# Performance work log

Measured on AMD Instinct MI355X. Metric: run time of the kernel, lower is better.

## Reference

```python
import jax, jax.numpy as jnp
import numpy as np

N = 50000        # nodes
E = 800000       # edges
F_IN = 32        # float features (x also carries 1 trailing cell-id column)
CELL_DIM = 16
NUM_CELLS = 854
C = 64           # out_channels
H0, H1 = 2, 1    # heads schedule for num_layers=2 -> [2, 1]
D_IN = F_IN + CELL_DIM  # 48, GAT input dim after cell embedding concat
NEG_SLOPE = 0.2  # PyG GATConv default negative_slope


def setup_inputs() -> dict:
    key = jax.random.key(0)
    ks = jax.random.split(key, 14)
    base = jax.random.normal(ks[0], (N, F_IN), jnp.float32)
    cell_ids = jax.random.randint(ks[1], (N,), 0, NUM_CELLS)
    x = jnp.concatenate([base, cell_ids.astype(jnp.float32)[:, None]], axis=1)
    edge_index = jax.random.randint(ks[2], (2, E), 0, N, dtype=jnp.int32)
    s = lambda f: 1.0 / np.sqrt(f)
    emb = jax.random.normal(ks[3], (NUM_CELLS, CELL_DIM), jnp.float32)
    W0 = jax.random.normal(ks[4], (D_IN, H0 * C), jnp.float32) * s(D_IN)
    a_src0 = jax.random.normal(ks[5], (H0, C), jnp.float32) * s(C)
    a_dst0 = jax.random.normal(ks[6], (H0, C), jnp.float32) * s(C)
    b0 = jnp.zeros((C,), jnp.float32)
    ln_g = jnp.ones((C,), jnp.float32)
    ln_b = jnp.zeros((C,), jnp.float32)
    W1 = jax.random.normal(ks[7], (C, H1 * C), jnp.float32) * s(C)
    a_src1 = jax.random.normal(ks[8], (H1, C), jnp.float32) * s(C)
    a_dst1 = jax.random.normal(ks[9], (H1, C), jnp.float32) * s(C)
    b1 = jnp.zeros((C,), jnp.float32)
    return {"x": x, "edge_index": edge_index, "emb": emb,
            "W0": W0, "a_src0": a_src0, "a_dst0": a_dst0, "b0": b0,
            "ln_g": ln_g, "ln_b": ln_b,
            "W1": W1, "a_src1": a_src1, "a_dst1": a_dst1, "b1": b1}


def gat_layer(h_in, src, dst, W, a_src, a_dst, b, heads):
    # h_in: [N, D]; src/dst: [E'] (self-loops already appended)
    h = (h_in @ W).reshape(N, heads, C)                 # [N, H, C]
    alpha_s = jnp.einsum('nhc,hc->nh', h, a_src)        # [N, H]
    alpha_d = jnp.einsum('nhc,hc->nh', h, a_dst)
    e = jax.nn.leaky_relu(alpha_s[src] + alpha_d[dst], NEG_SLOPE)  # [E', H]
    # segment softmax over incoming edges of each dst node
    m = jax.ops.segment_max(e, dst, num_segments=N)     # [N, H]
    ex = jnp.exp(e - m[dst])
    denom = jax.ops.segment_sum(ex, dst, num_segments=N)
    alpha = ex / denom[dst]                             # [E', H]
    msg = h[src] * alpha[:, :, None]                    # [E', H, C]
    out = jax.ops.segment_sum(msg, dst, num_segments=N) # [N, H, C]
    return out.mean(axis=1) + b                         # concat=False -> mean over heads


def layer_norm(x, g, b):
    mu = x.mean(-1, keepdims=True)
    var = ((x - mu) ** 2).mean(-1, keepdims=True)
    return (x - mu) * jax.lax.rsqrt(var + 1e-5) * g + b


def reference(x, edge_index, emb, W0, a_src0, a_dst0, b0, ln_g, ln_b,
              W1, a_src1, a_dst1, b1):
    base = x[:, :-1]
    cell_ids = x[:, -1].astype(jnp.int32)
    h = jnp.concatenate([base, emb[cell_ids]], axis=1)  # [N, 48]
    # add self-loops (PyG GATConv default add_self_loops=True)
    loop = jnp.arange(N, dtype=edge_index.dtype)
    src = jnp.concatenate([edge_index[0], loop])
    dst = jnp.concatenate([edge_index[1], loop])
    h = gat_layer(h, src, dst, W0, a_src0, a_dst0, b0, H0)
    h = jax.nn.elu(layer_norm(h, ln_g, ln_b))           # dropout is identity at eval
    h = gat_layer(h, src, dst, W1, a_src1, a_dst1, b1, H1)
    return h
```

## Files before the change

kernel.cpp:

```cpp
#include <hip/hip_runtime.h>
#include <hip/hip_bf16.h>

#define N_NODES 50000
#define N_EDGES 800000
#define E_TOT 850000
#define F_IN 32
#define CELL_DIM 16
#define D_IN 48
#define X_STRIDE 33
#define NUM_CELLS 854
#define NEG_SLOPE 0.2f
#define SCAN_BLOCKS 49
#define NODE0_BLOCKS 2048
#define HIST_BLOCKS 3125

typedef unsigned int uint;
typedef unsigned short ushort;

static __device__ __forceinline__ uint f2b(float f) {
  uint x = __float_as_uint(f);
  return (x + 0x7fffu + ((x >> 16) & 1u)) >> 16;
}
static __device__ __forceinline__ float b2f_lo(uint w) { return __uint_as_float(w << 16); }
static __device__ __forceinline__ float b2f_hi(uint w) { return __uint_as_float(w & 0xffff0000u); }
static __device__ __forceinline__ float lrelu(float e) { return e > 0.f ? e : NEG_SLOPE * e; }


__global__ __launch_bounds__(256) void k_node0h(const float* __restrict__ x,
                                                const float* __restrict__ emb,
                                                const float* __restrict__ W0,
                                                const float* __restrict__ asrc,
                                                const float* __restrict__ adst,
                                                const int* __restrict__ ei,
                                                ushort* __restrict__ h0u,
                                                float* __restrict__ as0, float* __restrict__ ad0,
                                                int* __restrict__ deg) {
  int tid = threadIdx.x;
  if (blockIdx.x >= NODE0_BLOCKS) {
    int e = (blockIdx.x - NODE0_BLOCKS) * 256 + tid;
    if (e < N_EDGES) atomicAdd(&deg[ei[N_EDGES + e]], 1);
    return;
  }
  __shared__ float hin[8][48];
  int lane = tid & 63, wid = tid >> 6;
  int h = wid & 1;
  int q = wid >> 1;
  float w0r[D_IN];
#pragma unroll
  for (int k = 0; k < D_IN; ++k) w0r[k] = W0[k * 128 + h * 64 + lane];
  float av_s = asrc[h * 64 + lane], av_d = adst[h * 64 + lane];

  for (int g = blockIdx.x; g < N_NODES / 8; g += NODE0_BLOCKS) {
    int nb = g * 8;
#pragma unroll
    for (int j = 0; j < 2; ++j) {
      int loc = 2 * wid + j;
      int n = nb + loc;
      float t = 0.f;
      if (lane < 33) t = x[n * X_STRIDE + lane];
      int cid = (int)__shfl(t, 32, 64);
      cid = cid < 0 ? 0 : (cid >= NUM_CELLS ? NUM_CELLS - 1 : cid);
      if (lane >= 32 && lane < 48) t = emb[cid * CELL_DIM + (lane - 32)];
      if (lane < 48) hin[loc][lane] = t;
    }
    __syncthreads();
#pragma unroll
    for (int j = 0; j < 4; ++j) {
      int loc = 4 * q + j;
      int n = nb + loc;
      const float4* hp = (const float4*)hin[loc];
      float acc = 0.f;
#pragma unroll
      for (int k4 = 0; k4 < 12; ++k4) {
        float4 hh = hp[k4];
        acc = fmaf(hh.x, w0r[4 * k4 + 0], acc);
        acc = fmaf(hh.y, w0r[4 * k4 + 1], acc);
        acc = fmaf(hh.z, w0r[4 * k4 + 2], acc);
        acc = fmaf(hh.w, w0r[4 * k4 + 3], acc);
      }
      h0u[(n * 64 + lane) * 2 + h] = (ushort)f2b(acc);
      float sa = acc * av_s, sd = acc * av_d;
#pragma unroll
      for (int o = 32; o >= 1; o >>= 1) {
        sa += __shfl_xor(sa, o, 64);
        sd += __shfl_xor(sd, o, 64);
      }
      if (lane == 0) {
        as0[n * 2 + h] = sa;
        ad0[n * 2 + h] = sd;
      }
    }
    __syncthreads();
  }
}


__global__ __launch_bounds__(1024) void k_scan1(const int* __restrict__ deg, int* __restrict__ off,
                                                int* __restrict__ bsum) {
  __shared__ int ws[16];
  int tid = threadIdx.x;
  int lane = tid & 63, wid = tid >> 6;
  int i = blockIdx.x * 1024 + tid;
  int v = (i < N_NODES) ? deg[i] + 1 : 0;
  int sc = v;
#pragma unroll
  for (int o = 1; o < 64; o <<= 1) {
    int t = __shfl_up(sc, o, 64);
    if (lane >= o) sc += t;
  }
  if (lane == 63) ws[wid] = sc;
  __syncthreads();
  if (tid < 16) {
    int w = ws[tid];
    int s = w;
#pragma unroll
    for (int o = 1; o < 16; o <<= 1) {
      int t = __shfl_up(s, o, 64);
      if (tid >= o) s += t;
    }
    ws[tid] = s - w;
  }
  __syncthreads();
  int excl = sc - v + ws[wid];
  if (i < N_NODES) off[i] = excl;
  if (tid == 1023) bsum[blockIdx.x] = excl + v;
}

__global__ __launch_bounds__(1024) void k_scan23(int* __restrict__ off, int* __restrict__ ofs,
                                                 const int* __restrict__ bsum) {
  __shared__ int carry_s;
  int tid = threadIdx.x;
  if (tid < 64) {
    int v = (tid < SCAN_BLOCKS) ? bsum[tid] : 0;
    int s = v;
#pragma unroll
    for (int o = 1; o < 64; o <<= 1) {
      int t = __shfl_up(s, o, 64);
      if (tid >= o) s += t;
    }
    if (tid == (int)blockIdx.x) carry_s = s - v;
  }
  __syncthreads();
  int carry = carry_s;
  int i = blockIdx.x * 1024 + tid;
  if (i < N_NODES) {
    int v = off[i] + carry;
    off[i] = v;
    ofs[i] = v;
  }
  if (i == 0) off[N_NODES] = E_TOT;
}

__global__ __launch_bounds__(256) void k_scatter(const int* __restrict__ ei, int* __restrict__ ofs,
                                                 const int* __restrict__ off,
                                                 const float2* __restrict__ as0v,
                                                 const float2* __restrict__ ad0v,
                                                 uint2* __restrict__ ew) {
  int t = blockIdx.x * 256 + threadIdx.x;
  if (t < N_EDGES) {
    int s = ei[t], d = ei[N_EDGES + t];
    float2 a_s = as0v[s], a_d = ad0v[d];
    float w0 = __expf(lrelu(a_s.x + a_d.x));
    float w1 = __expf(lrelu(a_s.y + a_d.y));
    int p = atomicAdd(&ofs[d], 1);
    ew[p] = make_uint2((uint)s, f2b(w0) | (f2b(w1) << 16));
  } else if (t < N_EDGES + N_NODES) {
    int n = t - N_EDGES;
    int slot = off[n + 1] - 1;
    float2 a_s = as0v[n], a_d = ad0v[n];
    float w0 = __expf(lrelu(a_s.x + a_d.x));
    float w1 = __expf(lrelu(a_s.y + a_d.y));
    ew[slot] = make_uint2((uint)n, f2b(w0) | (f2b(w1) << 16));
  }
}


__global__ __launch_bounds__(256) void k_agg0(const int* __restrict__ off,
                                              const uint2* __restrict__ ew,
                                              const uint* __restrict__ h0p,
                                              const float* __restrict__ b0,
                                              const float* __restrict__ lng,
                                              const float* __restrict__ lnb,
                                              const float* __restrict__ W1,
                                              const float* __restrict__ asrc1,
                                              const float* __restrict__ adst1,
                                              ushort* __restrict__ h1b,
                                              float* __restrict__ as1, float* __restrict__ ad1) {
  int n = blockIdx.x * 4 + (threadIdx.x >> 6);
  int lane = threadIdx.x & 63;
  float acc0 = 0.f, acc1 = 0.f, den0 = 0.f, den1 = 0.f;
  int i0 = off[n], i1 = off[n + 1];
  int i = i0;
  for (; i + 7 < i1; i += 8) {
    uint2 r[8];
    uint h[8];
#pragma unroll
    for (int j = 0; j < 8; ++j) r[j] = ew[i + j];
#pragma unroll
    for (int j = 0; j < 8; ++j) h[j] = h0p[r[j].x * 64 + lane];
#pragma unroll
    for (int j = 0; j < 8; ++j) {
      float w;
      w = b2f_lo(r[j].y); acc0 += w * b2f_lo(h[j]); den0 += w;
      w = b2f_hi(r[j].y); acc1 += w * b2f_hi(h[j]); den1 += w;
    }
  }
  for (; i + 3 < i1; i += 4) {
    uint2 r[4];
    uint h[4];
#pragma unroll
    for (int j = 0; j < 4; ++j) r[j] = ew[i + j];
#pragma unroll
    for (int j = 0; j < 4; ++j) h[j] = h0p[r[j].x * 64 + lane];
#pragma unroll
    for (int j = 0; j < 4; ++j) {
      float w;
      w = b2f_lo(r[j].y); acc0 += w * b2f_lo(h[j]); den0 += w;
      w = b2f_hi(r[j].y); acc1 += w * b2f_hi(h[j]); den1 += w;
    }
  }
  for (; i < i1; ++i) {
    uint2 r = ew[i];
    uint h = h0p[r.x * 64 + lane];
    float w;
    w = b2f_lo(r.y); acc0 += w * b2f_lo(h); den0 += w;
    w = b2f_hi(r.y); acc1 += w * b2f_hi(h); den1 += w;
  }
  float v = 0.5f * (acc0 / den0 + acc1 / den1) + b0[lane];
  float mu = v;
#pragma unroll
  for (int o = 32; o >= 1; o >>= 1) mu += __shfl_xor(mu, o, 64);
  mu *= (1.0f / 64.0f);
  float d = v - mu;
  float vr = d * d;
#pragma unroll
  for (int o = 32; o >= 1; o >>= 1) vr += __shfl_xor(vr, o, 64);
  vr *= (1.0f / 64.0f);
  float y = d * rsqrtf(vr + 1e-5f) * lng[lane] + lnb[lane];
  y = y > 0.f ? y : expm1f(y);
  float h1v = 0.f;
#pragma unroll
  for (int k = 0; k < 64; ++k) {
    float yk = __shfl(y, k, 64);
    h1v += yk * W1[k * 64 + lane];
  }
  h1b[n * 64 + lane] = (ushort)f2b(h1v);
  float sa = h1v * asrc1[lane];
  float sdv = h1v * adst1[lane];
#pragma unroll
  for (int o = 32; o >= 1; o >>= 1) {
    sa += __shfl_xor(sa, o, 64);
    sdv += __shfl_xor(sdv, o, 64);
  }
  if (lane == 0) {
    as1[n] = sa;
    ad1[n] = sdv;
  }
}


__global__ __launch_bounds__(256) void k_agg1(const int* __restrict__ off,
                                              const uint2* __restrict__ ew,
                                              const ushort* __restrict__ h1b,
                                              const float* __restrict__ as1,
                                              const float* __restrict__ ad1,
                                              const float* __restrict__ b1,
                                              float* __restrict__ out) {
  int n = blockIdx.x * 4 + (threadIdx.x >> 6);
  int lane = threadIdx.x & 63;
  float adv = ad1[n];
  float acc = 0.f, den = 0.f;
  int i0 = off[n], i1 = off[n + 1];
  int i = i0;
  for (; i + 7 < i1; i += 8) {
    uint s[8];
    float a[8];
    uint h[8];
#pragma unroll
    for (int j = 0; j < 8; ++j) s[j] = ew[i + j].x;
#pragma unroll
    for (int j = 0; j < 8; ++j) a[j] = as1[s[j]];
#pragma unroll
    for (int j = 0; j < 8; ++j) h[j] = h1b[s[j] * 64 + lane];
#pragma unroll
    for (int j = 0; j < 8; ++j) {
      float w = __expf(lrelu(a[j] + adv));
      acc += w * __uint_as_float(h[j] << 16);
      den += w;
    }
  }
  for (; i + 3 < i1; i += 4) {
    uint s[4];
    float a[4];
    uint h[4];
#pragma unroll
    for (int j = 0; j < 4; ++j) s[j] = ew[i + j].x;
#pragma unroll
    for (int j = 0; j < 4; ++j) a[j] = as1[s[j]];
#pragma unroll
    for (int j = 0; j < 4; ++j) h[j] = h1b[s[j] * 64 + lane];
#pragma unroll
    for (int j = 0; j < 4; ++j) {
      float w = __expf(lrelu(a[j] + adv));
      acc += w * __uint_as_float(h[j] << 16);
      den += w;
    }
  }
  for (; i < i1; ++i) {
    uint s = ew[i].x;
    float w = __expf(lrelu(as1[s] + adv));
    acc += w * __uint_as_float((uint)h1b[s * 64 + lane] << 16);
    den += w;
  }
  out[n * 64 + lane] = acc / den + b1[lane];
}


extern "C" void kernel_launch(void* const* d_in, const int* in_sizes, int n_in,
                              void* d_out, int out_size, void* d_ws, size_t ws_size,
                              hipStream_t stream) {
  const float* x    = (const float*)d_in[0];
  const int*   ei   = (const int*)d_in[1];
  const float* emb  = (const float*)d_in[2];
  const float* W0   = (const float*)d_in[3];
  const float* as0w = (const float*)d_in[4];
  const float* ad0w = (const float*)d_in[5];
  const float* b0   = (const float*)d_in[6];
  const float* lng  = (const float*)d_in[7];
  const float* lnb  = (const float*)d_in[8];
  const float* W1   = (const float*)d_in[9];
  const float* as1w = (const float*)d_in[10];
  const float* ad1w = (const float*)d_in[11];
  const float* b1   = (const float*)d_in[12];
  float* out = (float*)d_out;

  uint2* ew  = (uint2*)d_ws;
  float* as0 = (float*)(ew + E_TOT);
  float* ad0 = as0 + N_NODES * 2;
  float* as1 = ad0 + N_NODES * 2;
  float* ad1 = as1 + N_NODES;
  uint* h0p = (uint*)(ad1 + N_NODES);
  ushort* h1b = (ushort*)(h0p + N_NODES * 64);
  int* deg  = (int*)(h1b + N_NODES * 64);
  int* off  = deg + N_NODES;
  int* ofs  = off + N_NODES + 1;
  int* bsum = ofs + N_NODES;

  hipMemsetAsync(deg, 0, N_NODES * sizeof(int), stream);
  k_node0h<<<NODE0_BLOCKS + HIST_BLOCKS, 256, 0, stream>>>(x, emb, W0, as0w, ad0w, ei,
                                                           (ushort*)h0p, as0, ad0, deg);
  k_scan1<<<SCAN_BLOCKS, 1024, 0, stream>>>(deg, off, bsum);
  k_scan23<<<SCAN_BLOCKS, 1024, 0, stream>>>(off, ofs, bsum);
  k_scatter<<<(N_EDGES + N_NODES + 255) / 256, 256, 0, stream>>>(ei, ofs, off, (const float2*)as0,
                                                                 (const float2*)ad0, ew);
  k_agg0<<<N_NODES / 4, 256, 0, stream>>>(off, ew, h0p, b0, lng, lnb, W1, as1w, ad1w,
                                          h1b, as1, ad1);
  k_agg1<<<N_NODES / 4, 256, 0, stream>>>(off, ew, h1b, as1, ad1, b1, out);
}
```

Baseline: 271.5 us.

## Split each node's edge aggregation across two wavefronts and use LDS for W1 matvec

Each node's incoming-edge range in both aggregation kernels is now split between two wavefronts, with partial sums combined through shared memory after a block barrier. The aim is more memory-level parallelism for the gather-bound loops, which have an average degree of about 17. In k_agg0 the 64-step shuffle matvec with W1 is replaced by an LDS-broadcast float4 read of y with four independent FMA chains. The cost is a __syncthreads, extra LDS traffic, and half the waves sitting idle during the epilogue.

```diff
diff --git a/kernel.cpp b/kernel.cpp
--- a/kernel.cpp
+++ b/kernel.cpp
@@ -175,7 +175,7 @@
 }
 
 
-__global__ __launch_bounds__(256) void k_agg0(const int* __restrict__ off,
+__global__ __launch_bounds__(512) void k_agg0(const int* __restrict__ off,
                                               const uint2* __restrict__ ew,
                                               const uint* __restrict__ h0p,
                                               const float* __restrict__ b0,
@@ -186,12 +186,20 @@
                                               const float* __restrict__ adst1,
                                               ushort* __restrict__ h1b,
                                               float* __restrict__ as1, float* __restrict__ ad1) {
-  int n = blockIdx.x * 4 + (threadIdx.x >> 6);
-  int lane = threadIdx.x & 63;
+  __shared__ float part[4][4][64];
+  __shared__ float yb[4][64];
+  int tid = threadIdx.x;
+  int lane = tid & 63, wid = tid >> 6;
+  int nl = wid >> 1;
+  int half = wid & 1;
+  int n = blockIdx.x * 4 + nl;
   float acc0 = 0.f, acc1 = 0.f, den0 = 0.f, den1 = 0.f;
   int i0 = off[n], i1 = off[n + 1];
-  int i = i0;
-  for (; i + 7 < i1; i += 8) {
+  int mid = i0 + ((i1 - i0 + 1) >> 1);
+  int lo = half ? mid : i0;
+  int hi = half ? i1 : mid;
+  int i = lo;
+  for (; i + 7 < hi; i += 8) {
     uint2 r[8];
     uint h[8];
 #pragma unroll
@@ -205,7 +213,7 @@
       w = b2f_hi(r[j].y); acc1 += w * b2f_hi(h[j]); den1 += w;
     }
   }
-  for (; i + 3 < i1; i += 4) {
+  for (; i + 3 < hi; i += 4) {
     uint2 r[4];
     uint h[4];
 #pragma unroll
@@ -219,13 +227,26 @@
       w = b2f_hi(r[j].y); acc1 += w * b2f_hi(h[j]); den1 += w;
     }
   }
-  for (; i < i1; ++i) {
+  for (; i < hi; ++i) {
     uint2 r = ew[i];
     uint h = h0p[r.x * 64 + lane];
     float w;
     w = b2f_lo(r.y); acc0 += w * b2f_lo(h); den0 += w;
     w = b2f_hi(r.y); acc1 += w * b2f_hi(h); den1 += w;
   }
+  if (half) {
+    part[nl][0][lane] = acc0;
+    part[nl][1][lane] = acc1;
+    part[nl][2][lane] = den0;
+    part[nl][3][lane] = den1;
+  }
+  __syncthreads();
+  if (half) return;
+  acc0 += part[nl][0][lane];
+  acc1 += part[nl][1][lane];
+  den0 += part[nl][2][lane];
+  den1 += part[nl][3][lane];
+
   float v = 0.5f * (acc0 / den0 + acc1 / den1) + b0[lane];
   float mu = v;
 #pragma unroll
@@ -238,12 +259,18 @@
   vr *= (1.0f / 64.0f);
   float y = d * rsqrtf(vr + 1e-5f) * lng[lane] + lnb[lane];
   y = y > 0.f ? y : expm1f(y);
-  float h1v = 0.f;
-#pragma unroll
-  for (int k = 0; k < 64; ++k) {
-    float yk = __shfl(y, k, 64);
-    h1v += yk * W1[k * 64 + lane];
-  }
+  yb[nl][lane] = y;
+  const float4* yp = (const float4*)yb[nl];
+  float p0 = 0.f, p1 = 0.f, p2 = 0.f, p3 = 0.f;
+#pragma unroll
+  for (int k4 = 0; k4 < 16; ++k4) {
+    float4 yy = yp[k4];
+    p0 = fmaf(yy.x, W1[(4 * k4 + 0) * 64 + lane], p0);
+    p1 = fmaf(yy.y, W1[(4 * k4 + 1) * 64 + lane], p1);
+    p2 = fmaf(yy.z, W1[(4 * k4 + 2) * 64 + lane], p2);
+    p3 = fmaf(yy.w, W1[(4 * k4 + 3) * 64 + lane], p3);
+  }
+  float h1v = (p0 + p1) + (p2 + p3);
   h1b[n * 64 + lane] = (ushort)f2b(h1v);
   float sa = h1v * asrc1[lane];
   float sdv = h1v * adst1[lane];
@@ -259,20 +286,27 @@
 }
 
 
-__global__ __launch_bounds__(256) void k_agg1(const int* __restrict__ off,
+__global__ __launch_bounds__(512) void k_agg1(const int* __restrict__ off,
                                               const uint2* __restrict__ ew,
                                               const ushort* __restrict__ h1b,
                                               const float* __restrict__ as1,
                                               const float* __restrict__ ad1,
                                               const float* __restrict__ b1,
                                               float* __restrict__ out) {
-  int n = blockIdx.x * 4 + (threadIdx.x >> 6);
-  int lane = threadIdx.x & 63;
+  __shared__ float part[4][2][64];
+  int tid = threadIdx.x;
+  int lane = tid & 63, wid = tid >> 6;
+  int nl = wid >> 1;
+  int half = wid & 1;
+  int n = blockIdx.x * 4 + nl;
   float adv = ad1[n];
   float acc = 0.f, den = 0.f;
   int i0 = off[n], i1 = off[n + 1];
-  int i = i0;
-  for (; i + 7 < i1; i += 8) {
+  int mid = i0 + ((i1 - i0 + 1) >> 1);
+  int lo = half ? mid : i0;
+  int hi = half ? i1 : mid;
+  int i = lo;
+  for (; i + 7 < hi; i += 8) {
     uint s[8];
     float a[8];
     uint h[8];
@@ -289,7 +323,7 @@
       den += w;
     }
   }
-  for (; i + 3 < i1; i += 4) {
+  for (; i + 3 < hi; i += 4) {
     uint s[4];
     float a[4];
     uint h[4];
@@ -306,12 +340,20 @@
       den += w;
     }
   }
-  for (; i < i1; ++i) {
+  for (; i < hi; ++i) {
     uint s = ew[i].x;
     float w = __expf(lrelu(as1[s] + adv));
     acc += w * __uint_as_float((uint)h1b[s * 64 + lane] << 16);
     den += w;
   }
+  if (half) {
+    part[nl][0][lane] = acc;
+    part[nl][1][lane] = den;
+  }
+  __syncthreads();
+  if (half) return;
+  acc += part[nl][0][lane];
+  den += part[nl][1][lane];
   out[n * 64 + lane] = acc / den + b1[lane];
 }
 
@@ -353,7 +395,7 @@
   k_scan23<<<SCAN_BLOCKS, 1024, 0, stream>>>(off, ofs, bsum);
   k_scatter<<<(N_EDGES + N_NODES + 255) / 256, 256, 0, stream>>>(ei, ofs, off, (const float2*)as0,
                                                                  (const float2*)ad0, ew);
-  k_agg0<<<N_NODES / 4, 256, 0, stream>>>(off, ew, h0p, b0, lng, lnb, W1, as1w, ad1w,
+  k_agg0<<<N_NODES / 4, 512, 0, stream>>>(off, ew, h0p, b0, lng, lnb, W1, as1w, ad1w,
                                           h1b, as1, ad1);
-  k_agg1<<<N_NODES / 4, 256, 0, stream>>>(off, ew, h1b, as1, ad1, b1, out);
-}
+  k_agg1<<<N_NODES / 4, 512, 0, stream>>>(off, ew, h1b, as1, ad1, b1, out);
+}
```

New measurement: 313.4 us. 15.4% more time.
